# Kernel optimization log

Hardware: AMD Instinct MI355X
Metric: run time of the kernel (lower is better)

## Reference

```python
import jax, jax.numpy as jnp
import numpy as np

TEMPERATURE = 0.1
EPS = 1e-12  # tf.math.l2_normalize epsilon

BATCH = 512
DIM = 256
QUEUE = 65536


def l2_normalize(x, axis=1):
    sq = jnp.sum(x * x, axis=axis, keepdims=True)
    return x * jax.lax.rsqrt(jnp.maximum(sq, EPS))


def setup_inputs() -> dict:
    key = jax.random.key(0)
    k1, k2, k3 = jax.random.split(key, 3)
    projections_1 = jax.random.normal(k1, (BATCH, DIM), dtype=jnp.float32)
    projections_2 = jax.random.normal(k2, (BATCH, DIM), dtype=jnp.float32)
    feature_queue = l2_normalize(jax.random.normal(k3, (QUEUE, DIM), dtype=jnp.float32), axis=1)
    return {"projections_1": projections_1, "projections_2": projections_2, "feature_queue": feature_queue}


def nearest_neighbour(projections, feature_queue):
    # [B, Q] similarity vs the memory queue, 1-NN retrieval + gather
    support_similarities = jnp.einsum('bd,qd->bq', projections, feature_queue)
    nn_idx = jnp.argmax(support_similarities, axis=1)
    nn_projections = feature_queue[nn_idx]  # [B, D]
    # straight-through: forward value is nn, gradient flows to projections
    return projections + jax.lax.stop_gradient(nn_projections - projections)


def reference(projections_1, projections_2, feature_queue):
    p1 = l2_normalize(projections_1, axis=1)
    p2 = l2_normalize(projections_2, axis=1)

    nn1 = nearest_neighbour(p1, feature_queue)
    nn2 = nearest_neighbour(p2, feature_queue)

    s_1_2_1 = jnp.einsum('bd,cd->bc', nn1, p2) / TEMPERATURE
    s_1_2_2 = jnp.einsum('bd,cd->bc', p2, nn1) / TEMPERATURE
    s_2_1_1 = jnp.einsum('bd,cd->bc', nn2, p1) / TEMPERATURE
    s_2_1_2 = jnp.einsum('bd,cd->bc', p1, nn2) / TEMPERATURE

    logits = jnp.concatenate([s_1_2_1, s_1_2_2, s_2_1_1, s_2_1_2], axis=0)  # [4B, B]
    batch = p1.shape[0]
    labels = jnp.tile(jnp.arange(batch), 4)  # [4B]

    # sparse categorical crossentropy from logits
    logp = jax.nn.log_softmax(logits, axis=-1)
    loss = -logp[jnp.arange(4 * batch), labels]  # [4B]

    # FIFO queue update (normalized projections_1 pushed in front)
    new_queue = jnp.concatenate([p1, feature_queue[:-batch]], axis=0)
    return loss, new_queue
```

## Files before the change

kernel.cpp:

```cpp
#include <hip/hip_runtime.h>
#include <stdint.h>


#define BATCH  512
#define DIM    256
#define QUEUE  65536
#define MROWS  1024
#define NGRP   2048
#define MARGIN 0.01f

typedef short bf16x8 __attribute__((ext_vector_type(8)));
typedef float f32x4  __attribute__((ext_vector_type(4)));

__device__ __forceinline__ unsigned int mono_f32(float f) {
    unsigned int u = __float_as_uint(f);
    return (u & 0x80000000u) ? ~u : (u | 0x80000000u);
}
__device__ __forceinline__ float unmono_f32(unsigned int m) {
    unsigned int u = (m & 0x80000000u) ? (m ^ 0x80000000u) : ~m;
    return __uint_as_float(u);
}
__device__ __forceinline__ unsigned short f2bf(float f) {
    unsigned int u = __float_as_uint(f);
    return (unsigned short)((u + 0x7fffu + ((u >> 16) & 1u)) >> 16);
}

__global__ __launch_bounds__(256)
void k01_prep(const float* __restrict__ queue, float* __restrict__ outq,
              char* __restrict__ Qbf,
              const float* __restrict__ p1, const float* __restrict__ p2,
              float* __restrict__ Pn, float* __restrict__ PnT,
              unsigned short* __restrict__ PhiF,
              unsigned int* __restrict__ rowmaxU, unsigned long long* __restrict__ rowfinal)
{
    const int bid = blockIdx.x;
    const int t = threadIdx.x;

    if (bid >= 256) {
        const int b0 = bid - 256;
        const int n0 = b0 * 32;
        const f32x4* qsrc = (const f32x4*)(queue + (size_t)n0 * DIM);
        f32x4* qdst = (f32x4*)(outq + (size_t)(n0 + BATCH) * DIM);
        char* tile = Qbf + (size_t)(b0 >> 1) * 32768;

        f32x4 va[8];
        #pragma unroll
        for (int it = 0; it < 4; ++it) {
            const int L = it * 256 + t;
            const int r = L >> 5, c16 = L & 31;
            va[2 * it]     = qsrc[(size_t)r * 64 + c16 * 2];
            va[2 * it + 1] = qsrc[(size_t)r * 64 + c16 * 2 + 1];
        }
        __builtin_amdgcn_sched_barrier(0);
        #pragma unroll
        for (int it = 0; it < 4; ++it) {
            const int L = it * 256 + t;
            const int r = L >> 5, c16 = L & 31;
            f32x4 v0 = va[2 * it], v1 = va[2 * it + 1];
            if (n0 + r < QUEUE - BATCH) {
                qdst[(size_t)r * 64 + c16 * 2]     = v0;
                qdst[(size_t)r * 64 + c16 * 2 + 1] = v1;
            }
            bf16x8 bb;
            bb[0] = (short)f2bf(v0.x); bb[1] = (short)f2bf(v0.y);
            bb[2] = (short)f2bf(v0.z); bb[3] = (short)f2bf(v0.w);
            bb[4] = (short)f2bf(v1.x); bb[5] = (short)f2bf(v1.y);
            bb[6] = (short)f2bf(v1.z); bb[7] = (short)f2bf(v1.w);
            const int rr = ((b0 & 1) << 5) + r;
            *(bf16x8*)(tile + rr * 512 + ((c16 ^ (rr & 31)) << 4)) = bb;
        }
    } else {
        const int sub = t >> 6, lane = t & 63;
        const int r = bid * 4 + sub;
        if (lane == 0) {
            rowmaxU[r] = 0u;
            rowfinal[r] = 0ull;
        }
        const float* src = (r < BATCH) ? p1 : p2;
        const int row = (r < BATCH) ? r : r - BATCH;
        float4 v = ((const float4*)(src + (size_t)row * DIM))[lane];
        float sq = v.x*v.x + v.y*v.y + v.z*v.z + v.w*v.w;
        #pragma unroll
        for (int off = 32; off; off >>= 1) sq += __shfl_xor(sq, off, 64);
        sq = fmaxf(sq, 1e-12f);
        float s = rsqrtf(sq);
        s = s * (1.5f - 0.5f * sq * s * s);
        v.x *= s; v.y *= s; v.z *= s; v.w *= s;
        ((float4*)(Pn + (size_t)r * DIM))[lane] = v;
        const int k = lane * 4;
        PnT[(size_t)(k + 0) * MROWS + r] = v.x;
        PnT[(size_t)(k + 1) * MROWS + r] = v.y;
        PnT[(size_t)(k + 2) * MROWS + r] = v.z;
        PnT[(size_t)(k + 3) * MROWS + r] = v.w;
        short4 b;
        b.x = (short)f2bf(v.x); b.y = (short)f2bf(v.y);
        b.z = (short)f2bf(v.z); b.w = (short)f2bf(v.w);
        {
            const int c = lane >> 1;
            const int idx = ((r >> 4) * 8 + (c >> 2)) * 64 + (c & 3) * 16 + (r & 15);
            *(short4*)((char*)PhiF + (size_t)idx * 16 + (lane & 1) * 8) = b;
        }
        if (r < BATCH) ((float4*)(outq + (size_t)r * DIM))[lane] = v;
    }
}

__device__ __forceinline__ void k2_stage_half(const char* __restrict__ src,
                                              char* dst, int t)
{
    #pragma unroll
    for (int it = 0; it < 4; ++it) {
        const int L = it * 256 + t;
        __builtin_amdgcn_global_load_lds(
            (const __attribute__((address_space(1))) unsigned int*)(src + (size_t)L * 16),
            (__attribute__((address_space(3))) unsigned int*)(dst + L * 16), 16, 0, 0);
    }
}

__global__ __launch_bounds__(256, 2)
void k2_mfma(const unsigned short* __restrict__ PhiF, const char* __restrict__ Qbf,
             float* __restrict__ cand, unsigned int* __restrict__ rowmaxU)
{
    __shared__ __align__(16) char Bs[4][16384];
    const int bid = blockIdx.x;
    const int c = (bid >> 5) * 8 + (bid & 7);
    const int s = (bid >> 3) & 3;
    const int t  = threadIdx.x;
    const int w  = t >> 6, lane = t & 63;
    const int lr = lane & 15, q = lane >> 4;
    const int mbase = s * 256 + w * 64;
    const char* chunkbase = Qbf + (size_t)(c * 4) * 32768;

    bf16x8 pfr[4][8];
    {
        const char* Pw = (const char*)PhiF;
        const int mt16b = mbase >> 4;
        #pragma unroll
        for (int mj = 0; mj < 4; ++mj)
            #pragma unroll
            for (int ks = 0; ks < 8; ++ks)
                pfr[mj][ks] = *(const bf16x8*)(Pw + ((size_t)((mt16b + mj) * 8 + ks) * 64 + lane) * 16);
    }

    k2_stage_half(chunkbase,         Bs[0], t);
    k2_stage_half(chunkbase + 16384, Bs[1], t);

    float rowmx[4] = {-1e30f, -1e30f, -1e30f, -1e30f};

    #pragma unroll
    for (int h = 0; h < 8; ++h) {
        if (h + 2 < 8)
            k2_stage_half(chunkbase + (size_t)(h + 2) * 16384, Bs[(h + 2) & 3], t);

        if (h == 0)      asm volatile("s_waitcnt vmcnt(8)"  ::: "memory");
        else if (h <= 5) asm volatile("s_waitcnt vmcnt(12)" ::: "memory");
        else if (h == 6) asm volatile("s_waitcnt vmcnt(8)"  ::: "memory");
        else             asm volatile("s_waitcnt vmcnt(4)"  ::: "memory");
        __builtin_amdgcn_s_barrier();
        __builtin_amdgcn_sched_barrier(0);

        const char* Bsb = Bs[h & 3];
        f32x4 acc[2][4];
        #pragma unroll
        for (int i = 0; i < 2; ++i)
            #pragma unroll
            for (int j = 0; j < 4; ++j) acc[i][j] = (f32x4){0.f, 0.f, 0.f, 0.f};

        #pragma unroll
        for (int ks = 0; ks < 8; ++ks) {
            bf16x8 qf[2];
            #pragma unroll
            for (int ni = 0; ni < 2; ++ni) {
                const int rl = ni * 16 + lr;
                const int c16 = ks * 4 + q;
                qf[ni] = *(const bf16x8*)(Bsb + rl * 512 + ((c16 ^ rl) << 4));
            }
            #pragma unroll
            for (int ni = 0; ni < 2; ++ni)
                #pragma unroll
                for (int mj = 0; mj < 4; ++mj)
                    acc[ni][mj] = __builtin_amdgcn_mfma_f32_16x16x32_bf16(qf[ni], pfr[mj][ks], acc[ni][mj], 0, 0, 0);
        }

        #pragma unroll
        for (int mj = 0; mj < 4; ++mj) {
            f32x4 va = acc[0][mj], vb = acc[1][mj];
            float mx = fmaxf(fmaxf(fmaxf(va[0], va[1]), fmaxf(va[2], va[3])),
                             fmaxf(fmaxf(vb[0], vb[1]), fmaxf(vb[2], vb[3])));
            mx = fmaxf(mx, __shfl_xor(mx, 16, 64));
            mx = fmaxf(mx, __shfl_xor(mx, 32, 64));
            rowmx[mj] = fmaxf(rowmx[mj], mx);
            if (q == 0)
                cand[(size_t)(c * 8 + h) * MROWS + (mbase + mj * 16 + lr)] = mx;
        }
        __builtin_amdgcn_s_barrier();
        __builtin_amdgcn_sched_barrier(0);
    }

    if (q == 0) {
        #pragma unroll
        for (int mj = 0; mj < 4; ++mj)
            atomicMax(rowmaxU + mbase + mj * 16 + lr, mono_f32(rowmx[mj]));
    }
}

__global__ __launch_bounds__(256)
void k2cd(const float* __restrict__ cand, const unsigned int* __restrict__ rowmaxU,
          const float* __restrict__ Pn, const float* __restrict__ queue,
          unsigned long long* __restrict__ rowfinal)
{
    __shared__ unsigned int hits[4096];
    __shared__ int nhits;
    const int t = threadIdx.x;
    if (t == 0) nhits = 0;
    __syncthreads();

    {
        const int ml = t & 63, gs = t >> 6;
        const int mc = blockIdx.x & 15, gc = blockIdx.x >> 4;
        const int m  = mc * 64 + ml;
        const int g0 = gc * 64 + gs * 16;
        const float thr = unmono_f32(rowmaxU[m]) - MARGIN;
        #pragma unroll 8
        for (int j = 0; j < 16; ++j) {
            if (cand[(size_t)(g0 + j) * MROWS + m] >= thr) {
                int p = atomicAdd(&nhits, 1);
                hits[p] = ((unsigned int)m << 16) | (unsigned int)(g0 + j);
            }
        }
    }
    __syncthreads();

    const int n = nhits;
    const int w = t >> 6, lane = t & 63;
    const int col_l = lane & 31, half = lane >> 5;
    for (int p = w; p < n; p += 4) {
        const unsigned int pr = hits[p];
        const int row = pr >> 16, g = pr & 0xffff;
        const int col = g * 32 + col_l;
        const float4* qp = (const float4*)(queue + (size_t)col * DIM + half * 128);
        const float4* pp = (const float4*)(Pn + (size_t)row * DIM + half * 128);
        float4 sv = {0.f, 0.f, 0.f, 0.f};
        #pragma unroll 8
        for (int j = 0; j < 32; ++j) {
            float4 a = pp[j], b = qp[j];
            sv.x = fmaf(a.x, b.x, sv.x); sv.y = fmaf(a.y, b.y, sv.y);
            sv.z = fmaf(a.z, b.z, sv.z); sv.w = fmaf(a.w, b.w, sv.w);
        }
        float s = (sv.x + sv.y) + (sv.z + sv.w);
        s += __shfl_xor(s, 32, 64);
        unsigned long long best = ((unsigned long long)mono_f32(s) << 32)
                                | (unsigned int)(65535 - col);
        #pragma unroll
        for (int off = 1; off <= 16; off <<= 1) {
            unsigned long long o = __shfl_xor(best, off, 64);
            best = best > o ? best : o;
        }
        if (lane == 0) atomicMax(rowfinal + row, best);
    }
}

__global__ void k3_sim(const unsigned long long* __restrict__ rowfinal,
                       const float* __restrict__ queue,
                       const float* __restrict__ PnT, float* __restrict__ S)
{
    const int b  = blockIdx.x;
    const int rb = (b >> 1) * 4;
    const int ch = b & 1;
    const int tid = threadIdx.x;
    const int which = (rb < BATCH) ? 0 : 1;
    const int colbase = which ? 0 : BATCH;
    const int col = colbase + ch * 256 + tid;
    __shared__ float nnv[4][DIM];
    #pragma unroll
    for (int j = 0; j < 4; ++j) {
        const int idx = 65535 - (int)(rowfinal[rb + j] & 0xFFFFull);
        nnv[j][tid] = queue[(size_t)idx * DIM + tid];
    }
    __syncthreads();
    float acc[4];
    #pragma unroll
    for (int j = 0; j < 4; ++j) acc[j] = 0.f;
    for (int k4 = 0; k4 < 64; ++k4) {
        float4 nv[4];
        #pragma unroll
        for (int j = 0; j < 4; ++j) nv[j] = ((const float4*)nnv[j])[k4];
        #pragma unroll
        for (int kk = 0; kk < 4; ++kk) {
            const int k = k4 * 4 + kk;
            const float v0 = PnT[(size_t)k * MROWS + col];
            #pragma unroll
            for (int j = 0; j < 4; ++j) {
                const float nj = ((const float*)&nv[j])[kk];
                acc[j] = fmaf(nj, v0, acc[j]);
            }
        }
    }
    const int i0 = rb & (BATCH - 1);
    float* Sout = S + (size_t)which * (BATCH * BATCH);
    #pragma unroll
    for (int j = 0; j < 4; ++j)
        Sout[(size_t)(i0 + j) * BATCH + ch * 256 + tid] = acc[j] * 10.0f;
}

__global__ void k4_loss(const float* __restrict__ S, float* __restrict__ loss)
{
    const int r = blockIdx.x;
    const int tid = threadIdx.x;
    const int grp = r >> 9;
    const int i = r & 511;
    const float* M = S + (size_t)(grp >> 1) * (BATCH * BATCH);
    float x0, x1;
    if (!(grp & 1)) { x0 = M[(size_t)i * BATCH + tid];  x1 = M[(size_t)i * BATCH + tid + 256]; }
    else            { x0 = M[(size_t)tid * BATCH + i];  x1 = M[(size_t)(tid + 256) * BATCH + i]; }
    const float diag = M[(size_t)i * BATCH + i];
    float mx = fmaxf(x0, x1);
    #pragma unroll
    for (int off = 1; off < 64; off <<= 1) mx = fmaxf(mx, __shfl_xor(mx, off, 64));
    __shared__ float redm[4], reds[4];
    if ((tid & 63) == 0) redm[tid >> 6] = mx;
    __syncthreads();
    mx = fmaxf(fmaxf(redm[0], redm[1]), fmaxf(redm[2], redm[3]));
    float e = __expf(x0 - mx) + __expf(x1 - mx);
    #pragma unroll
    for (int off = 1; off < 64; off <<= 1) e += __shfl_xor(e, off, 64);
    if ((tid & 63) == 0) reds[tid >> 6] = e;
    __syncthreads();
    if (tid == 0)
        loss[r] = mx + logf(reds[0] + reds[1] + reds[2] + reds[3]) - diag;
}

extern "C" void kernel_launch(void* const* d_in, const int* in_sizes, int n_in,
                              void* d_out, int out_size, void* d_ws, size_t ws_size,
                              hipStream_t stream)
{
    const float* p1    = (const float*)d_in[0];
    const float* p2    = (const float*)d_in[1];
    const float* queue = (const float*)d_in[2];
    float* out  = (float*)d_out;
    float* loss = out;
    float* outq = out + 4 * BATCH;

    char* w = (char*)d_ws;
    float* cand = (float*)w;                               w += (size_t)NGRP * MROWS * 4;
    unsigned long long* rowfinal = (unsigned long long*)w; w += MROWS * 8;
    unsigned int* rowmaxU = (unsigned int*)w;              w += MROWS * 4;
    float* Pn  = (float*)w;                                w += (size_t)MROWS * DIM * 4;
    float* PnT = (float*)w;                                w += (size_t)MROWS * DIM * 4;
    unsigned short* PhiF = (unsigned short*)w;             w += (size_t)MROWS * DIM * 2;
    float* S = (float*)w;                                  w += (size_t)2 * BATCH * BATCH * 4;
    char* Qbf = w;

    hipLaunchKernelGGL(k01_prep,    dim3(256 + 2048), dim3(256), 0, stream,
                       queue, outq, Qbf, p1, p2, Pn, PnT, PhiF, rowmaxU, rowfinal);
    hipLaunchKernelGGL(k2_mfma,     dim3(1024), dim3(256), 0, stream, PhiF, Qbf, cand, rowmaxU);
    hipLaunchKernelGGL(k2cd,        dim3(512),  dim3(256), 0, stream, cand, rowmaxU, Pn, queue, rowfinal);
    hipLaunchKernelGGL(k3_sim,      dim3(512),  dim3(256), 0, stream, rowfinal, queue, PnT, S);
    hipLaunchKernelGGL(k4_loss,     dim3(4 * BATCH), dim3(256), 0, stream, S, loss);
}
```

Baseline: 212.9 us.

## Move FIFO queue copy out of prep into later small kernels

The fp32 queue-shift copy to the output is removed from the prep kernel, which now only converts the queue to bf16 tiles. The copy is split into extra blocks appended to the k2cd and k3_sim launches, so it runs alongside those latency-bound kernels and no longer lengthens the bandwidth-heavy prep pass. The trade-off is that queue data is read twice from memory, once in prep and once for the copy, and the later kernels get larger grids.

```diff
diff --git a/kernel.cpp b/kernel.cpp
--- a/kernel.cpp
+++ b/kernel.cpp
@@ -24,13 +24,20 @@
     unsigned int u = __float_as_uint(f);
     return (unsigned short)((u + 0x7fffu + ((u >> 16) & 1u)) >> 16);
 }
+__device__ __forceinline__ bf16x8 cvt8(f32x4 a, f32x4 b) {
+    bf16x8 r;
+    r[0] = (short)f2bf(a.x); r[1] = (short)f2bf(a.y);
+    r[2] = (short)f2bf(a.z); r[3] = (short)f2bf(a.w);
+    r[4] = (short)f2bf(b.x); r[5] = (short)f2bf(b.y);
+    r[6] = (short)f2bf(b.z); r[7] = (short)f2bf(b.w);
+    return r;
+}
 
 __global__ __launch_bounds__(256)
-void k01_prep(const float* __restrict__ queue, float* __restrict__ outq,
-              char* __restrict__ Qbf,
+void k01_prep(const float* __restrict__ queue, char* __restrict__ Qbf,
               const float* __restrict__ p1, const float* __restrict__ p2,
               float* __restrict__ Pn, float* __restrict__ PnT,
-              unsigned short* __restrict__ PhiF,
+              unsigned short* __restrict__ PhiF, float* __restrict__ outq,
               unsigned int* __restrict__ rowmaxU, unsigned long long* __restrict__ rowfinal)
 {
     const int bid = blockIdx.x;
@@ -40,34 +47,21 @@
         const int b0 = bid - 256;
         const int n0 = b0 * 32;
         const f32x4* qsrc = (const f32x4*)(queue + (size_t)n0 * DIM);
-        f32x4* qdst = (f32x4*)(outq + (size_t)(n0 + BATCH) * DIM);
         char* tile = Qbf + (size_t)(b0 >> 1) * 32768;
 
         f32x4 va[8];
+        #pragma unroll
+        for (int it = 0; it < 4; ++it) {
+            const int L = it * 256 + t;
+            va[2 * it]     = qsrc[(size_t)2 * L];
+            va[2 * it + 1] = qsrc[(size_t)2 * L + 1];
+        }
         #pragma unroll
         for (int it = 0; it < 4; ++it) {
             const int L = it * 256 + t;
             const int r = L >> 5, c16 = L & 31;
-            va[2 * it]     = qsrc[(size_t)r * 64 + c16 * 2];
-            va[2 * it + 1] = qsrc[(size_t)r * 64 + c16 * 2 + 1];
-        }
-        __builtin_amdgcn_sched_barrier(0);
-        #pragma unroll
-        for (int it = 0; it < 4; ++it) {
-            const int L = it * 256 + t;
-            const int r = L >> 5, c16 = L & 31;
-            f32x4 v0 = va[2 * it], v1 = va[2 * it + 1];
-            if (n0 + r < QUEUE - BATCH) {
-                qdst[(size_t)r * 64 + c16 * 2]     = v0;
-                qdst[(size_t)r * 64 + c16 * 2 + 1] = v1;
-            }
-            bf16x8 bb;
-            bb[0] = (short)f2bf(v0.x); bb[1] = (short)f2bf(v0.y);
-            bb[2] = (short)f2bf(v0.z); bb[3] = (short)f2bf(v0.w);
-            bb[4] = (short)f2bf(v1.x); bb[5] = (short)f2bf(v1.y);
-            bb[6] = (short)f2bf(v1.z); bb[7] = (short)f2bf(v1.w);
             const int rr = ((b0 & 1) << 5) + r;
-            *(bf16x8*)(tile + rr * 512 + ((c16 ^ (rr & 31)) << 4)) = bb;
+            *(bf16x8*)(tile + rr * 512 + ((c16 ^ (rr & 31)) << 4)) = cvt8(va[2 * it], va[2 * it + 1]);
         }
     } else {
         const int sub = t >> 6, lane = t & 63;
@@ -206,17 +200,32 @@
 __global__ __launch_bounds__(256)
 void k2cd(const float* __restrict__ cand, const unsigned int* __restrict__ rowmaxU,
           const float* __restrict__ Pn, const float* __restrict__ queue,
-          unsigned long long* __restrict__ rowfinal)
-{
+          unsigned long long* __restrict__ rowfinal, float* __restrict__ outq)
+{
+    const int bid = blockIdx.x;
+    const int t = threadIdx.x;
+
+    if (bid >= 512) {
+        const int b0 = bid - 512;
+        const int n0 = b0 * 32;
+        const f32x4* qsrc = (const f32x4*)(queue + (size_t)n0 * DIM);
+        f32x4* qdst = (f32x4*)(outq + (size_t)(n0 + BATCH) * DIM);
+        #pragma unroll
+        for (int it = 0; it < 8; ++it) {
+            const int idx = it * 256 + t;
+            qdst[idx] = qsrc[idx];
+        }
+        return;
+    }
+
     __shared__ unsigned int hits[4096];
     __shared__ int nhits;
-    const int t = threadIdx.x;
     if (t == 0) nhits = 0;
     __syncthreads();
 
     {
         const int ml = t & 63, gs = t >> 6;
-        const int mc = blockIdx.x & 15, gc = blockIdx.x >> 4;
+        const int mc = bid & 15, gc = bid >> 4;
         const int m  = mc * 64 + ml;
         const int g0 = gc * 64 + gs * 16;
         const float thr = unmono_f32(rowmaxU[m]) - MARGIN;
@@ -261,12 +270,29 @@
 
 __global__ void k3_sim(const unsigned long long* __restrict__ rowfinal,
                        const float* __restrict__ queue,
-                       const float* __restrict__ PnT, float* __restrict__ S)
-{
-    const int b  = blockIdx.x;
+                       const float* __restrict__ PnT, float* __restrict__ S,
+                       float* __restrict__ outq)
+{
+    const int bid = blockIdx.x;
+    const int tid = threadIdx.x;
+
+    if (bid >= 512) {
+        const int b0 = 1024 + (bid - 512);
+        const int n0 = b0 * 32;
+        const f32x4* qsrc = (const f32x4*)(queue + (size_t)n0 * DIM);
+        f32x4* qdst = (f32x4*)(outq + (size_t)(n0 + BATCH) * DIM);
+        #pragma unroll
+        for (int it = 0; it < 8; ++it) {
+            const int idx = it * 256 + tid;
+            const int r = idx >> 6;
+            if (n0 + r < QUEUE - BATCH) qdst[idx] = qsrc[idx];
+        }
+        return;
+    }
+
+    const int b  = bid;
     const int rb = (b >> 1) * 4;
     const int ch = b & 1;
-    const int tid = threadIdx.x;
     const int which = (rb < BATCH) ? 0 : 1;
     const int colbase = which ? 0 : BATCH;
     const int col = colbase + ch * 256 + tid;
@@ -351,9 +377,10 @@
     char* Qbf = w;
 
     hipLaunchKernelGGL(k01_prep,    dim3(256 + 2048), dim3(256), 0, stream,
-                       queue, outq, Qbf, p1, p2, Pn, PnT, PhiF, rowmaxU, rowfinal);
+                       queue, Qbf, p1, p2, Pn, PnT, PhiF, outq, rowmaxU, rowfinal);
     hipLaunchKernelGGL(k2_mfma,     dim3(1024), dim3(256), 0, stream, PhiF, Qbf, cand, rowmaxU);
-    hipLaunchKernelGGL(k2cd,        dim3(512),  dim3(256), 0, stream, cand, rowmaxU, Pn, queue, rowfinal);
-    hipLaunchKernelGGL(k3_sim,      dim3(512),  dim3(256), 0, stream, rowfinal, queue, PnT, S);
+    hipLaunchKernelGGL(k2cd,        dim3(1536), dim3(256), 0, stream, cand, rowmaxU, Pn, queue,
+                       rowfinal, outq);
+    hipLaunchKernelGGL(k3_sim,      dim3(1536), dim3(256), 0, stream, rowfinal, queue, PnT, S, outq);
     hipLaunchKernelGGL(k4_loss,     dim3(4 * BATCH), dim3(256), 0, stream, S, loss);
 }
```

Result: no change. 211.7 us (-0.6%).
